# Optimization experiments

Measured on AMD Instinct MI355X. Metric: run time of the kernel, lower is better.

The kernel has to match this reference:

```python
import jax, jax.numpy as jnp
import numpy as np

CHUNK = 2048  # query points processed per step; bounds peak memory at [CHUNK, F, 3]


def _safe_div(num, den):
    den_s = jnp.where(jnp.abs(den) > 1e-12, den, 1.0)
    return num / den_s


def _closest_point_on_triangle(p, a, b, c):
    """Ericson's region-based closest point on triangle.
    p: [n,1,3], a/b/c: [1,F,3] -> returns [n,F,3]."""
    ab = b - a
    ac = c - a
    ap = p - a
    d1 = jnp.sum(ab * ap, -1)
    d2 = jnp.sum(ac * ap, -1)
    bp = p - b
    d3 = jnp.sum(ab * bp, -1)
    d4 = jnp.sum(ac * bp, -1)
    cpv = p - c
    d5 = jnp.sum(ab * cpv, -1)
    d6 = jnp.sum(ac * cpv, -1)
    vc = d1 * d4 - d3 * d2
    vb = d5 * d2 - d1 * d6
    va = d3 * d6 - d5 * d4
    v_ab = jnp.clip(_safe_div(d1, d1 - d3), 0.0, 1.0)
    w_ac = jnp.clip(_safe_div(d2, d2 - d6), 0.0, 1.0)
    w_bc = jnp.clip(_safe_div(d4 - d3, (d4 - d3) + (d5 - d6)), 0.0, 1.0)
    denom = va + vb + vc
    v = _safe_div(vb, denom)
    w = _safe_div(vc, denom)
    res = a + ab * v[..., None] + ac * w[..., None]  # face interior
    m_bc = (va <= 0) & ((d4 - d3) >= 0) & ((d5 - d6) >= 0)
    m_ac = (vb <= 0) & (d2 >= 0) & (d6 <= 0)
    m_ab = (vc <= 0) & (d1 >= 0) & (d3 <= 0)
    m_c = (d6 >= 0) & (d5 <= d6)
    m_b = (d3 >= 0) & (d4 <= d3)
    m_a = (d1 <= 0) & (d2 <= 0)
    res = jnp.where(m_bc[..., None], b + w_bc[..., None] * (c - b), res)
    res = jnp.where(m_ac[..., None], a + w_ac[..., None] * ac, res)
    res = jnp.where(m_ab[..., None], a + v_ab[..., None] * ab, res)
    res = jnp.where(m_c[..., None], c, res)
    res = jnp.where(m_b[..., None], b, res)
    res = jnp.where(m_a[..., None], a, res)
    return res


def _query_one_batch(tris, pts):
    # tris: [F,3,3], pts: [Q,3]
    a, b, c = tris[:, 0], tris[:, 1], tris[:, 2]

    def chunk_fn(pc):  # pc: [CHUNK,3]
        cp = _closest_point_on_triangle(pc[:, None, :], a[None], b[None], c[None])  # [CHUNK,F,3]
        d2 = jnp.sum((pc[:, None, :] - cp) ** 2, -1)  # [CHUNK,F] squared distances
        dist = jnp.min(d2, axis=-1)
        idx = jnp.argmin(d2, axis=-1)
        closest = jnp.take_along_axis(cp, idx[:, None, None], axis=1)[:, 0]
        return dist, closest, idx.astype(jnp.int32)

    Q = pts.shape[0]
    pts_c = pts.reshape(Q // CHUNK, CHUNK, 3)
    dist, closest, idx = jax.lax.map(chunk_fn, pts_c)
    return dist.reshape(Q), closest.reshape(Q, 3), idx.reshape(Q)


def setup_inputs() -> dict:
    key = jax.random.key(0)
    k1, k2 = jax.random.split(key)
    triangles = jax.random.normal(k1, (2, 4096, 3, 3), dtype=jnp.float32)
    points = jax.random.normal(k2, (2, 16384, 3), dtype=jnp.float32)
    return {"triangles": triangles, "points": points}


def reference(triangles, points):
    # distances are SQUARED point-to-mesh distances, matching the CUDA kernel
    distances, closest_points, closest_faces = jax.vmap(_query_one_batch)(triangles, points)
    return distances, closest_points, closest_faces
```

## Files before the change

kernel.cpp:

```cpp
#include <hip/hip_runtime.h>
#include <math.h>

namespace {

typedef float v2f __attribute__((ext_vector_type(2)));

constexpr int B = 2;
constexpr int F = 4096;
constexpr int Q = 16384;
constexpr int NP = B * Q;
constexpr int BLOCK = 256;
constexpr int P4 = 4;

constexpr int OFF_DIST = 0;
constexpr int OFF_CP = NP;
constexpr int OFF_FACE = 4 * NP;


__device__ __forceinline__ float safediv(float num, float den) {
  #pragma clang fp contract(off)
  float d = (fabsf(den) > 1e-12f) ? den : 1.0f;
  return num / d;
}

__device__ __forceinline__ float clamp01(float x) {
  return fminf(fmaxf(x, 0.0f), 1.0f);
}

__device__ __forceinline__ void closest_pt(
    float px, float py, float pz,
    float ax, float ay, float az,
    float bx, float by, float bz,
    float cx, float cy, float cz,
    float& rx, float& ry, float& rz) {
  #pragma clang fp contract(off)
  float abx = bx - ax, aby = by - ay, abz = bz - az;
  float acx = cx - ax, acy = cy - ay, acz = cz - az;
  float apx = px - ax, apy = py - ay, apz = pz - az;
  float d1 = (abx * apx + aby * apy) + abz * apz;
  float d2 = (acx * apx + acy * apy) + acz * apz;
  float bpx = px - bx, bpy = py - by, bpz = pz - bz;
  float d3 = (abx * bpx + aby * bpy) + abz * bpz;
  float d4 = (acx * bpx + acy * bpy) + acz * bpz;
  float cpx = px - cx, cpy = py - cy, cpz = pz - cz;
  float d5 = (abx * cpx + aby * cpy) + abz * cpz;
  float d6 = (acx * cpx + acy * cpy) + acz * cpz;

  float vc = d1 * d4 - d3 * d2;
  float vb = d5 * d2 - d1 * d6;
  float va = d3 * d6 - d5 * d4;

  float v_ab = clamp01(safediv(d1, d1 - d3));
  float w_ac = clamp01(safediv(d2, d2 - d6));
  float w_bc = clamp01(safediv(d4 - d3, (d4 - d3) + (d5 - d6)));

  float denom = (va + vb) + vc;
  float v = safediv(vb, denom);
  float w = safediv(vc, denom);

  float ox = ax + abx * v + acx * w;
  float oy = ay + aby * v + acy * w;
  float oz = az + abz * v + acz * w;

  bool m_bc = (va <= 0.0f) && (d4 - d3 >= 0.0f) && (d5 - d6 >= 0.0f);
  bool m_ac = (vb <= 0.0f) && (d2 >= 0.0f) && (d6 <= 0.0f);
  bool m_ab = (vc <= 0.0f) && (d1 >= 0.0f) && (d3 <= 0.0f);
  bool m_c  = (d6 >= 0.0f) && (d5 <= d6);
  bool m_b  = (d3 >= 0.0f) && (d4 <= d3);
  bool m_a  = (d1 <= 0.0f) && (d2 <= 0.0f);

  if (m_bc) { ox = bx + w_bc * (cx - bx); oy = by + w_bc * (cy - by); oz = bz + w_bc * (cz - bz); }
  if (m_ac) { ox = ax + w_ac * acx;       oy = ay + w_ac * acy;       oz = az + w_ac * acz; }
  if (m_ab) { ox = ax + v_ab * abx;       oy = ay + v_ab * aby;       oz = az + v_ab * abz; }
  if (m_c)  { ox = cx; oy = cy; oz = cz; }
  if (m_b)  { ox = bx; oy = by; oz = bz; }
  if (m_a)  { ox = ax; oy = ay; oz = az; }

  rx = ox; ry = oy; rz = oz;
}

__device__ __forceinline__ float exact_d2(
    float px, float py, float pz, const float* __restrict__ g ) {
  #pragma clang fp contract(off)
  float rx, ry, rz;
  closest_pt(px, py, pz,
             g[0], g[1], g[2], g[3], g[4], g[5], g[6], g[7], g[8],
             rx, ry, rz);
  float dx = px - rx, dy = py - ry, dz = pz - rz;
  return (dx * dx + dy * dy) + dz * dz;
}


__device__ __forceinline__ unsigned umin2(unsigned a, unsigned b) { return a < b ? a : b; }
__device__ __forceinline__ unsigned umax2(unsigned a, unsigned b) { return a > b ? a : b; }

__device__ __forceinline__ void ins2(unsigned k, unsigned& K1, unsigned& K2) {
  unsigned t = umax2(K1, k);
  K1 = umin2(K1, k);
  K2 = umin2(K2, t);
}

__device__ __forceinline__ void ins8(unsigned k,
    unsigned& K1, unsigned& K2, unsigned& K3, unsigned& K4,
    unsigned& K5, unsigned& K6, unsigned& K7, unsigned& K8) {
  unsigned t;
  t = umax2(K1, k); K1 = umin2(K1, k);
  k = t; t = umax2(K2, k); K2 = umin2(K2, k);
  k = t; t = umax2(K3, k); K3 = umin2(K3, k);
  k = t; t = umax2(K4, k); K4 = umin2(K4, k);
  k = t; t = umax2(K5, k); K5 = umin2(K5, k);
  k = t; t = umax2(K6, k); K6 = umin2(K6, k);
  k = t; t = umax2(K7, k); K7 = umin2(K7, k);
  K8 = umin2(K8, t);
}


__device__ __forceinline__ unsigned fin_one(
    float dint, float tabm, float tacm, float tbcm,
    float td1, float td2, float ap2m, float bp2, float t43d,
    float va, float vb, float vc,
    float aa, float bb, float cc, float pp, int gidx) {
  float tab = __builtin_amdgcn_fmed3f(tabm, 0.0f, 1.0f);
  float sab = fmaf(-tab, fmaf(-tab, aa, td1), ap2m);
  float tac = __builtin_amdgcn_fmed3f(tacm, 0.0f, 1.0f);
  float sac = fmaf(-tac, fmaf(-tac, bb, td2), ap2m);
  float tbc = __builtin_amdgcn_fmed3f(tbcm, 0.0f, 1.0f);
  float sbc = fmaf(-tbc, fmaf(-tbc, cc, t43d), bp2);
  float dseg = fminf(fminf(sab, sac), sbc);
  float mv   = fminf(fminf(va, vb), vc);
  float d = (mv > 0.0f) ? dint : dseg;
  d = fmaxf(d + pp, 0.0f);
  return (__float_as_uint(d) & 0xFFFFF000u) | (unsigned)gidx;
}

template <int NC>
__global__ __launch_bounds__(BLOCK, 4) void bvh_screen4(
    const float* __restrict__ tris,
    const float* __restrict__ pts,
    uint2* __restrict__ keys) {
  constexpr int CFL = F / NC;
  __shared__ float4 s_rec[5 * CFL];

  constexpr int BPB = (Q / P4) / BLOCK;
  const int batch = blockIdx.x / BPB;
  const int j = (blockIdx.x % BPB) * BLOCK + threadIdx.x;
  const int chunk = blockIdx.y;
  const int tri0 = chunk * CFL;
  const float* tb = tris + (size_t)batch * F * 9;

  for (int t = threadIdx.x; t < CFL; t += BLOCK) {
    const float* g = tb + (size_t)(tri0 + t) * 9;
    float ax = g[0], ay = g[1], az = g[2];
    float abx = g[3] - ax, aby = g[4] - ay, abz = g[5] - az;
    float acx = g[6] - ax, acy = g[7] - ay, acz = g[8] - az;
    float aa   = abx * abx + aby * aby + abz * abz;
    float bb   = acx * acx + acy * acy + acz * acz;
    float abac = abx * acx + aby * acy + abz * acz;
    float bcx = acx - abx, bcy = acy - aby, bcz = acz - abz;
    float cc   = bcx * bcx + bcy * bcy + bcz * bcz;
    float nx = aby * acz - abz * acy;
    float ny = abz * acx - abx * acz;
    float nz = abx * acy - aby * acx;
    float n2 = nx * nx + ny * ny + nz * nz;
    float raa = (aa > 1e-12f) ? 1.0f / aa : 1.0f;
    float rbb = (bb > 1e-12f) ? 1.0f / bb : 1.0f;
    float rcc = (cc > 1e-12f) ? 1.0f / cc : 1.0f;
    float rdn = (n2 > 1e-12f) ? 1.0f / n2 : 1.0f;
    float c1 = -(ax * abx + ay * aby + az * abz);
    float c2 = -(ax * acx + ay * acy + az * acz);
    float caa2 = ax * ax + ay * ay + az * az;
    s_rec[0 * CFL + t] = make_float4(abx, aby, abz, c1);
    s_rec[1 * CFL + t] = make_float4(acx, acy, acz, c2);
    s_rec[2 * CFL + t] = make_float4(-2.0f * ax, -2.0f * ay, -2.0f * az, caa2);
    s_rec[3 * CFL + t] = make_float4(aa, bb, abac, cc);
    s_rec[4 * CFL + t] = make_float4(raa, rbb, rcc, rdn);
  }
  __syncthreads();

  const int p0 = batch * Q + j;
  float px0 = pts[(p0          ) * 3 + 0], py0 = pts[(p0          ) * 3 + 1], pz0 = pts[(p0          ) * 3 + 2];
  float px1 = pts[(p0 + Q/4    ) * 3 + 0], py1 = pts[(p0 + Q/4    ) * 3 + 1], pz1 = pts[(p0 + Q/4    ) * 3 + 2];
  float px2 = pts[(p0 + Q/2    ) * 3 + 0], py2 = pts[(p0 + Q/2    ) * 3 + 1], pz2 = pts[(p0 + Q/2    ) * 3 + 2];
  float px3 = pts[(p0 + 3*(Q/4)) * 3 + 0], py3 = pts[(p0 + 3*(Q/4)) * 3 + 1], pz3 = pts[(p0 + 3*(Q/4)) * 3 + 2];

  const v2f pxA = {px0, px1}, pyA = {py0, py1}, pzA = {pz0, pz1};
  const v2f pxB = {px2, px3}, pyB = {py2, py3}, pzB = {pz2, pz3};
  const float pp0 = px0*px0 + py0*py0 + pz0*pz0;
  const float pp1 = px1*px1 + py1*py1 + pz1*pz1;
  const float pp2 = px2*px2 + py2*py2 + pz2*pz2;
  const float pp3 = px3*px3 + py3*py3 + pz3*pz3;

  unsigned A1 = ~0u, A2 = ~0u, Bk1 = ~0u, Bk2 = ~0u;
  unsigned C1 = ~0u, C2 = ~0u, D1 = ~0u, D2 = ~0u;

  {
    #pragma clang fp contract(fast)
    for (int t = 0; t < CFL; ++t) {
      const float4 R0 = s_rec[0 * CFL + t];
      const float4 R1 = s_rec[1 * CFL + t];
      const float4 R2 = s_rec[2 * CFL + t];
      const float4 R3 = s_rec[3 * CFL + t];
      const float4 R4 = s_rec[4 * CFL + t];
      const int gidx = tri0 + t;

      {
        v2f d1   = pxA * R0.x + pyA * R0.y + pzA * R0.z + R0.w;
        v2f d2   = pxA * R1.x + pyA * R1.y + pzA * R1.z + R1.w;
        v2f ap2m = pxA * R2.x + pyA * R2.y + pzA * R2.z + R2.w;
        v2f d3 = d1 - R3.x, d6 = d2 - R3.y, d4 = d2 - R3.z, d5 = d1 - R3.z;
        v2f t43 = d4 - d3;
        v2f va = d3 * d6 - d5 * d4;
        v2f vb = d5 * d2 - d1 * d6;
        v2f vc = d1 * d4 - d3 * d2;
        v2f td1 = d1 + d1, td2 = d2 + d2;
        v2f v = vb * R4.w, w = vc * R4.w;
        v2f h1 = v * R3.x + (w * R3.z - td1);
        v2f h2 = w * R3.y + (v * R3.z - td2);
        v2f dint = ap2m + (v * h1 + w * h2);
        v2f tabm = d1 * R4.x, tacm = d2 * R4.y, tbcm = t43 * R4.z;
        v2f bp2 = (ap2m - td1) + R3.x;
        v2f t43d = t43 + t43;
        ins2(fin_one(dint.x, tabm.x, tacm.x, tbcm.x, td1.x, td2.x, ap2m.x,
                     bp2.x, t43d.x, va.x, vb.x, vc.x,
                     R3.x, R3.y, R3.w, pp0, gidx), A1, A2);
        ins2(fin_one(dint.y, tabm.y, tacm.y, tbcm.y, td1.y, td2.y, ap2m.y,
                     bp2.y, t43d.y, va.y, vb.y, vc.y,
                     R3.x, R3.y, R3.w, pp1, gidx), Bk1, Bk2);
      }
      {
        v2f d1   = pxB * R0.x + pyB * R0.y + pzB * R0.z + R0.w;
        v2f d2   = pxB * R1.x + pyB * R1.y + pzB * R1.z + R1.w;
        v2f ap2m = pxB * R2.x + pyB * R2.y + pzB * R2.z + R2.w;
        v2f d3 = d1 - R3.x, d6 = d2 - R3.y, d4 = d2 - R3.z, d5 = d1 - R3.z;
        v2f t43 = d4 - d3;
        v2f va = d3 * d6 - d5 * d4;
        v2f vb = d5 * d2 - d1 * d6;
        v2f vc = d1 * d4 - d3 * d2;
        v2f td1 = d1 + d1, td2 = d2 + d2;
        v2f v = vb * R4.w, w = vc * R4.w;
        v2f h1 = v * R3.x + (w * R3.z - td1);
        v2f h2 = w * R3.y + (v * R3.z - td2);
        v2f dint = ap2m + (v * h1 + w * h2);
        v2f tabm = d1 * R4.x, tacm = d2 * R4.y, tbcm = t43 * R4.z;
        v2f bp2 = (ap2m - td1) + R3.x;
        v2f t43d = t43 + t43;
        ins2(fin_one(dint.x, tabm.x, tacm.x, tbcm.x, td1.x, td2.x, ap2m.x,
                     bp2.x, t43d.x, va.x, vb.x, vc.x,
                     R3.x, R3.y, R3.w, pp2, gidx), C1, C2);
        ins2(fin_one(dint.y, tabm.y, tacm.y, tbcm.y, td1.y, td2.y, ap2m.y,
                     bp2.y, t43d.y, va.y, vb.y, vc.y,
                     R3.x, R3.y, R3.w, pp3, gidx), D1, D2);
      }
    }
  }

  keys[(size_t)chunk * NP + p0            ] = make_uint2(A1, A2);
  keys[(size_t)chunk * NP + p0 + Q/4      ] = make_uint2(Bk1, Bk2);
  keys[(size_t)chunk * NP + p0 + Q/2      ] = make_uint2(C1, C2);
  keys[(size_t)chunk * NP + p0 + 3*(Q/4)  ] = make_uint2(D1, D2);
}


template <int NC>
__global__ __launch_bounds__(BLOCK) void bvh_finish2(
    const float* __restrict__ tris,
    const float* __restrict__ pts,
    const uint2* __restrict__ keys,
    float* __restrict__ out) {
  const int gpt = blockIdx.x * BLOCK + threadIdx.x;
  if (gpt >= NP) return;

  unsigned K1 = ~0u, K2 = ~0u, K3 = ~0u, K4 = ~0u;
  unsigned K5 = ~0u, K6 = ~0u, K7 = ~0u, K8 = ~0u;
  for (int c = 0; c < NC; ++c) {
    uint2 k = keys[(size_t)c * NP + gpt];
    ins8(k.x, K1, K2, K3, K4, K5, K6, K7, K8);
    ins8(k.y, K1, K2, K3, K4, K5, K6, K7, K8);
  }

  const int batch = gpt / Q;
  const float* tb = tris + (size_t)batch * F * 9;
  const float px = pts[gpt * 3 + 0];
  const float py = pts[gpt * 3 + 1];
  const float pz = pts[gpt * 3 + 2];

  float be = INFINITY;
  int bi = 0x7FFFFFFF;
  #define CAND(Kx) { int t_ = (int)(Kx & 0xFFFu); \
    float d_ = exact_d2(px, py, pz, tb + (size_t)t_ * 9); \
    if (d_ < be || (d_ == be && t_ < bi)) { be = d_; bi = t_; } }
  CAND(K1) CAND(K2) CAND(K3) CAND(K4) CAND(K5) CAND(K6) CAND(K7) CAND(K8)
  #undef CAND

  const float* tr = tb + (size_t)bi * 9;
  float rx, ry, rz;
  closest_pt(px, py, pz,
             tr[0], tr[1], tr[2], tr[3], tr[4], tr[5], tr[6], tr[7], tr[8],
             rx, ry, rz);

  out[OFF_DIST + gpt] = be;
  out[OFF_CP + gpt * 3 + 0] = rx;
  out[OFF_CP + gpt * 3 + 1] = ry;
  out[OFF_CP + gpt * 3 + 2] = rz;
  out[OFF_FACE + gpt] = (float)bi;
}


__device__ __forceinline__ float screen_d2_sc(
    float px, float py, float pz,
    float ax, float ay, float az,
    float abx, float aby, float abz,
    float acx, float acy, float acz,
    float aa, float bb, float abac,
    float raa, float rbb, float rcc, float rdn) {
  #pragma clang fp contract(fast)
  float apx = px - ax, apy = py - ay, apz = pz - az;
  float ap2 = fmaf(apx, apx, fmaf(apy, apy, apz * apz));
  float d1  = fmaf(apx, abx, fmaf(apy, aby, apz * abz));
  float d2  = fmaf(apx, acx, fmaf(apy, acy, apz * acz));
  float d3 = d1 - aa, d6 = d2 - bb, d4 = d2 - abac, d5 = d1 - abac;
  float t43 = d4 - d3, t56 = d5 - d6;
  float va = d3 * d6 - d5 * d4;
  float vb = d5 * d2 - d1 * d6;
  float vc = d1 * d4 - d3 * d2;
  float td1 = d1 + d1, td2 = d2 + d2;
  float v = vb * rdn, w = vc * rdn;
  float h1 = fmaf(v, aa, fmaf(w, abac, -td1));
  float h2 = fmaf(w, bb, fmaf(v, abac, -td2));
  float dint = ap2 + fmaf(v, h1, w * h2);
  float tab = __builtin_amdgcn_fmed3f(d1 * raa, 0.0f, 1.0f);
  float sab = fmaf(-tab, fmaf(-tab, aa, td1), ap2);
  float tac = __builtin_amdgcn_fmed3f(d2 * rbb, 0.0f, 1.0f);
  float sac = fmaf(-tac, fmaf(-tac, bb, td2), ap2);
  float cc  = t43 + t56;
  float bp2 = (ap2 - td1) + aa;
  float tbc = __builtin_amdgcn_fmed3f(t43 * rcc, 0.0f, 1.0f);
  float sbc = fmaf(-tbc, fmaf(-tbc, cc, t43 + t43), bp2);
  float dseg = fminf(fminf(sab, sac), sbc);
  float mv   = fminf(fminf(va, vb), vc);
  float d = (mv > 0.0f) ? dint : dseg;
  return fmaxf(d, 0.0f);
}

__device__ __forceinline__ void ins4c(unsigned key,
    unsigned& K1, unsigned& K2, unsigned& K3, unsigned& K4) {
  bool b1 = key < K1, b2 = key < K2, b3 = key < K3, b4 = key < K4;
  K4 = b3 ? K3 : (b4 ? key : K4);
  K3 = b2 ? K2 : (b3 ? key : K3);
  K2 = b1 ? K1 : (b2 ? key : K2);
  K1 = b1 ? key : K1;
}

__device__ __forceinline__ void tail4(
    const float* __restrict__ tb, int tri0,
    float px, float py, float pz,
    unsigned K1, unsigned K2, unsigned K3, unsigned K4,
    float& be, int& bi) {
  int c0 = (int)(K1 & 0x1FFu), c1 = (int)(K2 & 0x1FFu);
  int c2 = (int)(K3 & 0x1FFu), c3 = (int)(K4 & 0x1FFu);
  int tmp;
  if (c0 > c1) { tmp = c0; c0 = c1; c1 = tmp; }
  if (c2 > c3) { tmp = c2; c2 = c3; c3 = tmp; }
  if (c0 > c2) { tmp = c0; c0 = c2; c2 = tmp; }
  if (c1 > c3) { tmp = c1; c1 = c3; c3 = tmp; }
  if (c1 > c2) { tmp = c1; c1 = c2; c2 = tmp; }
  be = exact_d2(px, py, pz, tb + (size_t)(tri0 + c0) * 9);
  bi = c0;
  { float d = exact_d2(px, py, pz, tb + (size_t)(tri0 + c1) * 9);
    if (d < be) { be = d; bi = c1; } }
  { float d = exact_d2(px, py, pz, tb + (size_t)(tri0 + c2) * 9);
    if (d < be) { be = d; bi = c2; } }
  { float d = exact_d2(px, py, pz, tb + (size_t)(tri0 + c3) * 9);
    if (d < be) { be = d; bi = c3; } }
}

template <int NC>
__global__ __launch_bounds__(BLOCK, 4) void bvh_partial_p2(
    const float* __restrict__ tris,
    const float* __restrict__ pts,
    float* __restrict__ dbest,
    unsigned short* __restrict__ ibest) {
  constexpr int CFL = F / NC;
  __shared__ float4 s_rec[4 * CFL];

  constexpr int BPB = (Q / 2) / BLOCK;
  const int batch = blockIdx.x / BPB;
  const int j = (blockIdx.x % BPB) * BLOCK + threadIdx.x;
  const int chunk = blockIdx.y;
  const int tri0 = chunk * CFL;
  const float* tb = tris + (size_t)batch * F * 9;

  for (int t = threadIdx.x; t < CFL; t += BLOCK) {
    const float* g = tb + (size_t)(tri0 + t) * 9;
    float ax = g[0], ay = g[1], az = g[2];
    float abx = g[3] - ax, aby = g[4] - ay, abz = g[5] - az;
    float acx = g[6] - ax, acy = g[7] - ay, acz = g[8] - az;
    float aa   = abx * abx + aby * aby + abz * abz;
    float bb   = acx * acx + acy * acy + acz * acz;
    float abac = abx * acx + aby * acy + abz * acz;
    float bcx = acx - abx, bcy = acy - aby, bcz = acz - abz;
    float cc   = bcx * bcx + bcy * bcy + bcz * bcz;
    float nx = aby * acz - abz * acy;
    float ny = abz * acx - abx * acz;
    float nz = abx * acy - aby * acx;
    float n2 = nx * nx + ny * ny + nz * nz;
    float raa = (aa > 1e-12f) ? 1.0f / aa : 1.0f;
    float rbb = (bb > 1e-12f) ? 1.0f / bb : 1.0f;
    float rcc = (cc > 1e-12f) ? 1.0f / cc : 1.0f;
    float rdn = (n2 > 1e-12f) ? 1.0f / n2 : 1.0f;
    s_rec[0 * CFL + t] = make_float4(ax, ay, az, abx);
    s_rec[1 * CFL + t] = make_float4(aby, abz, acx, acy);
    s_rec[2 * CFL + t] = make_float4(acz, aa, bb, abac);
    s_rec[3 * CFL + t] = make_float4(raa, rbb, rcc, rdn);
  }
  __syncthreads();

  const int p0 = batch * Q + j;
  const int p1 = p0 + Q / 2;
  const float px0 = pts[p0 * 3 + 0], py0 = pts[p0 * 3 + 1], pz0 = pts[p0 * 3 + 2];
  const float px1 = pts[p1 * 3 + 0], py1 = pts[p1 * 3 + 1], pz1 = pts[p1 * 3 + 2];

  unsigned A1 = ~0u, A2 = ~0u, A3 = ~0u, A4 = ~0u;
  unsigned B1 = ~0u, B2 = ~0u, B3 = ~0u, B4 = ~0u;

  for (int t = 0; t < CFL; ++t) {
    const float4 R0 = s_rec[0 * CFL + t];
    const float4 R1 = s_rec[1 * CFL + t];
    const float4 R2 = s_rec[2 * CFL + t];
    const float4 R3 = s_rec[3 * CFL + t];
    float ax = R0.x, ay = R0.y, az = R0.z, abx = R0.w;
    float aby = R1.x, abz = R1.y, acx = R1.z, acy = R1.w;
    float acz = R2.x, aa = R2.y, bb = R2.z, abac = R2.w;
    float raa = R3.x, rbb = R3.y, rcc = R3.z, rdn = R3.w;

    float d0 = screen_d2_sc(px0, py0, pz0, ax, ay, az, abx, aby, abz,
                            acx, acy, acz, aa, bb, abac, raa, rbb, rcc, rdn);
    ins4c((__float_as_uint(d0) & 0xFFFFFE00u) | (unsigned)t, A1, A2, A3, A4);
    float d1 = screen_d2_sc(px1, py1, pz1, ax, ay, az, abx, aby, abz,
                            acx, acy, acz, aa, bb, abac, raa, rbb, rcc, rdn);
    ins4c((__float_as_uint(d1) & 0xFFFFFE00u) | (unsigned)t, B1, B2, B3, B4);
  }

  float be0, be1;
  int bi0, bi1;
  tail4(tb, tri0, px0, py0, pz0, A1, A2, A3, A4, be0, bi0);
  tail4(tb, tri0, px1, py1, pz1, B1, B2, B3, B4, be1, bi1);

  dbest[chunk * NP + p0] = be0;
  ibest[chunk * NP + p0] = (unsigned short)(tri0 + bi0);
  dbest[chunk * NP + p1] = be1;
  ibest[chunk * NP + p1] = (unsigned short)(tri0 + bi1);
}

template <int NC>
__global__ __launch_bounds__(BLOCK) void bvh_reduce(
    const float* __restrict__ tris,
    const float* __restrict__ pts,
    const float* __restrict__ dbest,
    const unsigned short* __restrict__ ibest,
    float* __restrict__ out) {
  const int gpt = blockIdx.x * BLOCK + threadIdx.x;
  if (gpt >= NP) return;

  float best = INFINITY;
  int bi = 0;
  for (int c = 0; c < NC; ++c) {
    float d = dbest[c * NP + gpt];
    if (d < best) { best = d; bi = ibest[c * NP + gpt]; }
  }

  const int batch = gpt / Q;
  const float px = pts[gpt * 3 + 0];
  const float py = pts[gpt * 3 + 1];
  const float pz = pts[gpt * 3 + 2];

  const float* tr = tris + ((size_t)batch * F + bi) * 9;
  float rx, ry, rz;
  closest_pt(px, py, pz,
             tr[0], tr[1], tr[2], tr[3], tr[4], tr[5], tr[6], tr[7], tr[8],
             rx, ry, rz);

  out[OFF_DIST + gpt] = best;
  out[OFF_CP + gpt * 3 + 0] = rx;
  out[OFF_CP + gpt * 3 + 1] = ry;
  out[OFF_CP + gpt * 3 + 2] = rz;
  out[OFF_FACE + gpt] = (float)bi;
}

}

extern "C" void kernel_launch(void* const* d_in, const int* in_sizes, int n_in,
                              void* d_out, int out_size, void* d_ws, size_t ws_size,
                              hipStream_t stream) {
  const float* tris = (const float*)d_in[0];
  const float* pts  = (const float*)d_in[1];
  float* out = (float*)d_out;

  dim3 grid2((NP + BLOCK - 1) / BLOCK);

  constexpr int NC = 32;
  constexpr size_t KEY_BYTES = (size_t)NC * NP * sizeof(uint2);

  if (ws_size >= KEY_BYTES) {
    uint2* keys = (uint2*)d_ws;
    const int gx = B * ((Q / P4) / BLOCK);
    bvh_screen4<NC><<<dim3(gx, NC), BLOCK, 0, stream>>>(tris, pts, keys);
    bvh_finish2<NC><<<grid2, BLOCK, 0, stream>>>(tris, pts, keys, out);
  } else {
    float* dbest = (float*)d_ws;
    unsigned short* ibest = (unsigned short*)((char*)d_ws + (size_t)8 * NP * sizeof(float));
    const int gx = B * ((Q / 2) / BLOCK);
    bvh_partial_p2<8><<<dim3(gx, 8), BLOCK, 0, stream>>>(tris, pts, dbest, ibest);
    bvh_reduce<8><<<grid2, BLOCK, 0, stream>>>(tris, pts, dbest, ibest, out);
  }
}
```

Baseline: 166.8 us.

## Precompute triangle records in a prep kernel and read them from global memory

Adds a bvh_prep kernel that computes the per-triangle records once for all batches and writes them to workspace. The screening kernel now reads these records directly from global memory with uniform loads instead of rebuilding them into shared memory in every block, and its loop is unrolled by 2. This removes the per-block setup work and the barrier, but costs an extra launch and per-iteration global or cache loads in place of LDS reads. The old two-point fallback path is replaced by the shared-memory screen kernel.

New measurement: 172.1 us. 3.2% more time.

```diff
diff --git a/kernel.cpp b/kernel.cpp
--- a/kernel.cpp
+++ b/kernel.cpp
@@ -114,7 +114,6 @@
   K8 = umin2(K8, t);
 }
 
-
 __device__ __forceinline__ unsigned fin_one(
     float dint, float tabm, float tacm, float tbcm,
     float td1, float td2, float ap2m, float bp2, float t43d,
@@ -133,49 +132,52 @@
   return (__float_as_uint(d) & 0xFFFFF000u) | (unsigned)gidx;
 }
 
+
+__global__ __launch_bounds__(BLOCK) void bvh_prep(
+    const float* __restrict__ tris, float4* __restrict__ rec) {
+  int i = blockIdx.x * BLOCK + threadIdx.x;
+  if (i >= B * F) return;
+  const float* g = tris + (size_t)i * 9;
+  float ax = g[0], ay = g[1], az = g[2];
+  float abx = g[3] - ax, aby = g[4] - ay, abz = g[5] - az;
+  float acx = g[6] - ax, acy = g[7] - ay, acz = g[8] - az;
+  float aa   = abx * abx + aby * aby + abz * abz;
+  float bb   = acx * acx + acy * acy + acz * acz;
+  float abac = abx * acx + aby * acy + abz * acz;
+  float bcx = acx - abx, bcy = acy - aby, bcz = acz - abz;
+  float cc   = bcx * bcx + bcy * bcy + bcz * bcz;
+  float nx = aby * acz - abz * acy;
+  float ny = abz * acx - abx * acz;
+  float nz = abx * acy - aby * acx;
+  float n2 = nx * nx + ny * ny + nz * nz;
+  float raa = (aa > 1e-12f) ? 1.0f / aa : 1.0f;
+  float rbb = (bb > 1e-12f) ? 1.0f / bb : 1.0f;
+  float rcc = (cc > 1e-12f) ? 1.0f / cc : 1.0f;
+  float rdn = (n2 > 1e-12f) ? 1.0f / n2 : 1.0f;
+  float c1 = -(ax * abx + ay * aby + az * abz);
+  float c2 = -(ax * acx + ay * acy + az * acz);
+  float caa2 = ax * ax + ay * ay + az * az;
+  float4* r = rec + (size_t)i * 5;
+  r[0] = make_float4(abx, aby, abz, c1);
+  r[1] = make_float4(acx, acy, acz, c2);
+  r[2] = make_float4(-2.0f * ax, -2.0f * ay, -2.0f * az, caa2);
+  r[3] = make_float4(aa, bb, abac, cc);
+  r[4] = make_float4(raa, rbb, rcc, rdn);
+}
+
+
 template <int NC>
-__global__ __launch_bounds__(BLOCK, 4) void bvh_screen4(
-    const float* __restrict__ tris,
+__global__ __launch_bounds__(BLOCK, 4) void bvh_screen_smem(
     const float* __restrict__ pts,
+    const float4* __restrict__ rec,
     uint2* __restrict__ keys) {
   constexpr int CFL = F / NC;
-  __shared__ float4 s_rec[5 * CFL];
-
   constexpr int BPB = (Q / P4) / BLOCK;
   const int batch = blockIdx.x / BPB;
   const int j = (blockIdx.x % BPB) * BLOCK + threadIdx.x;
   const int chunk = blockIdx.y;
   const int tri0 = chunk * CFL;
-  const float* tb = tris + (size_t)batch * F * 9;
-
-  for (int t = threadIdx.x; t < CFL; t += BLOCK) {
-    const float* g = tb + (size_t)(tri0 + t) * 9;
-    float ax = g[0], ay = g[1], az = g[2];
-    float abx = g[3] - ax, aby = g[4] - ay, abz = g[5] - az;
-    float acx = g[6] - ax, acy = g[7] - ay, acz = g[8] - az;
-    float aa   = abx * abx + aby * aby + abz * abz;
-    float bb   = acx * acx + acy * acy + acz * acz;
-    float abac = abx * acx + aby * acy + abz * acz;
-    float bcx = acx - abx, bcy = acy - aby, bcz = acz - abz;
-    float cc   = bcx * bcx + bcy * bcy + bcz * bcz;
-    float nx = aby * acz - abz * acy;
-    float ny = abz * acx - abx * acz;
-    float nz = abx * acy - aby * acx;
-    float n2 = nx * nx + ny * ny + nz * nz;
-    float raa = (aa > 1e-12f) ? 1.0f / aa : 1.0f;
-    float rbb = (bb > 1e-12f) ? 1.0f / bb : 1.0f;
-    float rcc = (cc > 1e-12f) ? 1.0f / cc : 1.0f;
-    float rdn = (n2 > 1e-12f) ? 1.0f / n2 : 1.0f;
-    float c1 = -(ax * abx + ay * aby + az * abz);
-    float c2 = -(ax * acx + ay * acy + az * acz);
-    float caa2 = ax * ax + ay * ay + az * az;
-    s_rec[0 * CFL + t] = make_float4(abx, aby, abz, c1);
-    s_rec[1 * CFL + t] = make_float4(acx, acy, acz, c2);
-    s_rec[2 * CFL + t] = make_float4(-2.0f * ax, -2.0f * ay, -2.0f * az, caa2);
-    s_rec[3 * CFL + t] = make_float4(aa, bb, abac, cc);
-    s_rec[4 * CFL + t] = make_float4(raa, rbb, rcc, rdn);
-  }
-  __syncthreads();
+  const float4* rb = rec + ((size_t)batch * F + tri0) * 5;
 
   const int p0 = batch * Q + j;
   float px0 = pts[(p0          ) * 3 + 0], py0 = pts[(p0          ) * 3 + 1], pz0 = pts[(p0          ) * 3 + 2];
@@ -195,12 +197,13 @@
 
   {
     #pragma clang fp contract(fast)
+    #pragma unroll 2
     for (int t = 0; t < CFL; ++t) {
-      const float4 R0 = s_rec[0 * CFL + t];
-      const float4 R1 = s_rec[1 * CFL + t];
-      const float4 R2 = s_rec[2 * CFL + t];
-      const float4 R3 = s_rec[3 * CFL + t];
-      const float4 R4 = s_rec[4 * CFL + t];
+      const float4 R0 = rb[t * 5 + 0];
+      const float4 R1 = rb[t * 5 + 1];
+      const float4 R2 = rb[t * 5 + 2];
+      const float4 R3 = rb[t * 5 + 3];
+      const float4 R4 = rb[t * 5 + 4];
       const int gidx = tri0 + t;
 
       {
@@ -306,84 +309,15 @@
 }
 
 
-__device__ __forceinline__ float screen_d2_sc(
-    float px, float py, float pz,
-    float ax, float ay, float az,
-    float abx, float aby, float abz,
-    float acx, float acy, float acz,
-    float aa, float bb, float abac,
-    float raa, float rbb, float rcc, float rdn) {
-  #pragma clang fp contract(fast)
-  float apx = px - ax, apy = py - ay, apz = pz - az;
-  float ap2 = fmaf(apx, apx, fmaf(apy, apy, apz * apz));
-  float d1  = fmaf(apx, abx, fmaf(apy, aby, apz * abz));
-  float d2  = fmaf(apx, acx, fmaf(apy, acy, apz * acz));
-  float d3 = d1 - aa, d6 = d2 - bb, d4 = d2 - abac, d5 = d1 - abac;
-  float t43 = d4 - d3, t56 = d5 - d6;
-  float va = d3 * d6 - d5 * d4;
-  float vb = d5 * d2 - d1 * d6;
-  float vc = d1 * d4 - d3 * d2;
-  float td1 = d1 + d1, td2 = d2 + d2;
-  float v = vb * rdn, w = vc * rdn;
-  float h1 = fmaf(v, aa, fmaf(w, abac, -td1));
-  float h2 = fmaf(w, bb, fmaf(v, abac, -td2));
-  float dint = ap2 + fmaf(v, h1, w * h2);
-  float tab = __builtin_amdgcn_fmed3f(d1 * raa, 0.0f, 1.0f);
-  float sab = fmaf(-tab, fmaf(-tab, aa, td1), ap2);
-  float tac = __builtin_amdgcn_fmed3f(d2 * rbb, 0.0f, 1.0f);
-  float sac = fmaf(-tac, fmaf(-tac, bb, td2), ap2);
-  float cc  = t43 + t56;
-  float bp2 = (ap2 - td1) + aa;
-  float tbc = __builtin_amdgcn_fmed3f(t43 * rcc, 0.0f, 1.0f);
-  float sbc = fmaf(-tbc, fmaf(-tbc, cc, t43 + t43), bp2);
-  float dseg = fminf(fminf(sab, sac), sbc);
-  float mv   = fminf(fminf(va, vb), vc);
-  float d = (mv > 0.0f) ? dint : dseg;
-  return fmaxf(d, 0.0f);
-}
-
-__device__ __forceinline__ void ins4c(unsigned key,
-    unsigned& K1, unsigned& K2, unsigned& K3, unsigned& K4) {
-  bool b1 = key < K1, b2 = key < K2, b3 = key < K3, b4 = key < K4;
-  K4 = b3 ? K3 : (b4 ? key : K4);
-  K3 = b2 ? K2 : (b3 ? key : K3);
-  K2 = b1 ? K1 : (b2 ? key : K2);
-  K1 = b1 ? key : K1;
-}
-
-__device__ __forceinline__ void tail4(
-    const float* __restrict__ tb, int tri0,
-    float px, float py, float pz,
-    unsigned K1, unsigned K2, unsigned K3, unsigned K4,
-    float& be, int& bi) {
-  int c0 = (int)(K1 & 0x1FFu), c1 = (int)(K2 & 0x1FFu);
-  int c2 = (int)(K3 & 0x1FFu), c3 = (int)(K4 & 0x1FFu);
-  int tmp;
-  if (c0 > c1) { tmp = c0; c0 = c1; c1 = tmp; }
-  if (c2 > c3) { tmp = c2; c2 = c3; c3 = tmp; }
-  if (c0 > c2) { tmp = c0; c0 = c2; c2 = tmp; }
-  if (c1 > c3) { tmp = c1; c1 = c3; c3 = tmp; }
-  if (c1 > c2) { tmp = c1; c1 = c2; c2 = tmp; }
-  be = exact_d2(px, py, pz, tb + (size_t)(tri0 + c0) * 9);
-  bi = c0;
-  { float d = exact_d2(px, py, pz, tb + (size_t)(tri0 + c1) * 9);
-    if (d < be) { be = d; bi = c1; } }
-  { float d = exact_d2(px, py, pz, tb + (size_t)(tri0 + c2) * 9);
-    if (d < be) { be = d; bi = c2; } }
-  { float d = exact_d2(px, py, pz, tb + (size_t)(tri0 + c3) * 9);
-    if (d < be) { be = d; bi = c3; } }
-}
-
 template <int NC>
-__global__ __launch_bounds__(BLOCK, 4) void bvh_partial_p2(
+__global__ __launch_bounds__(BLOCK, 4) void bvh_screen4(
     const float* __restrict__ tris,
     const float* __restrict__ pts,
-    float* __restrict__ dbest,
-    unsigned short* __restrict__ ibest) {
+    uint2* __restrict__ keys) {
   constexpr int CFL = F / NC;
-  __shared__ float4 s_rec[4 * CFL];
-
-  constexpr int BPB = (Q / 2) / BLOCK;
+  __shared__ float4 s_rec[5 * CFL];
+
+  constexpr int BPB = (Q / P4) / BLOCK;
   const int batch = blockIdx.x / BPB;
   const int j = (blockIdx.x % BPB) * BLOCK + threadIdx.x;
   const int chunk = blockIdx.y;
@@ -408,83 +342,97 @@
     float rbb = (bb > 1e-12f) ? 1.0f / bb : 1.0f;
     float rcc = (cc > 1e-12f) ? 1.0f / cc : 1.0f;
     float rdn = (n2 > 1e-12f) ? 1.0f / n2 : 1.0f;
-    s_rec[0 * CFL + t] = make_float4(ax, ay, az, abx);
-    s_rec[1 * CFL + t] = make_float4(aby, abz, acx, acy);
-    s_rec[2 * CFL + t] = make_float4(acz, aa, bb, abac);
-    s_rec[3 * CFL + t] = make_float4(raa, rbb, rcc, rdn);
+    float c1 = -(ax * abx + ay * aby + az * abz);
+    float c2 = -(ax * acx + ay * acy + az * acz);
+    float caa2 = ax * ax + ay * ay + az * az;
+    s_rec[0 * CFL + t] = make_float4(abx, aby, abz, c1);
+    s_rec[1 * CFL + t] = make_float4(acx, acy, acz, c2);
+    s_rec[2 * CFL + t] = make_float4(-2.0f * ax, -2.0f * ay, -2.0f * az, caa2);
+    s_rec[3 * CFL + t] = make_float4(aa, bb, abac, cc);
+    s_rec[4 * CFL + t] = make_float4(raa, rbb, rcc, rdn);
   }
   __syncthreads();
 
   const int p0 = batch * Q + j;
-  const int p1 = p0 + Q / 2;
-  const float px0 = pts[p0 * 3 + 0], py0 = pts[p0 * 3 + 1], pz0 = pts[p0 * 3 + 2];
-  const float px1 = pts[p1 * 3 + 0], py1 = pts[p1 * 3 + 1], pz1 = pts[p1 * 3 + 2];
-
-  unsigned A1 = ~0u, A2 = ~0u, A3 = ~0u, A4 = ~0u;
-  unsigned B1 = ~0u, B2 = ~0u, B3 = ~0u, B4 = ~0u;
-
-  for (int t = 0; t < CFL; ++t) {
-    const float4 R0 = s_rec[0 * CFL + t];
-    const float4 R1 = s_rec[1 * CFL + t];
-    const float4 R2 = s_rec[2 * CFL + t];
-    const float4 R3 = s_rec[3 * CFL + t];
-    float ax = R0.x, ay = R0.y, az = R0.z, abx = R0.w;
-    float aby = R1.x, abz = R1.y, acx = R1.z, acy = R1.w;
-    float acz = R2.x, aa = R2.y, bb = R2.z, abac = R2.w;
-    float raa = R3.x, rbb = R3.y, rcc = R3.z, rdn = R3.w;
-
-    float d0 = screen_d2_sc(px0, py0, pz0, ax, ay, az, abx, aby, abz,
-                            acx, acy, acz, aa, bb, abac, raa, rbb, rcc, rdn);
-    ins4c((__float_as_uint(d0) & 0xFFFFFE00u) | (unsigned)t, A1, A2, A3, A4);
-    float d1 = screen_d2_sc(px1, py1, pz1, ax, ay, az, abx, aby, abz,
-                            acx, acy, acz, aa, bb, abac, raa, rbb, rcc, rdn);
-    ins4c((__float_as_uint(d1) & 0xFFFFFE00u) | (unsigned)t, B1, B2, B3, B4);
+  float px0 = pts[(p0          ) * 3 + 0], py0 = pts[(p0          ) * 3 + 1], pz0 = pts[(p0          ) * 3 + 2];
+  float px1 = pts[(p0 + Q/4    ) * 3 + 0], py1 = pts[(p0 + Q/4    ) * 3 + 1], pz1 = pts[(p0 + Q/4    ) * 3 + 2];
+  float px2 = pts[(p0 + Q/2    ) * 3 + 0], py2 = pts[(p0 + Q/2    ) * 3 + 1], pz2 = pts[(p0 + Q/2    ) * 3 + 2];
+  float px3 = pts[(p0 + 3*(Q/4)) * 3 + 0], py3 = pts[(p0 + 3*(Q/4)) * 3 + 1], pz3 = pts[(p0 + 3*(Q/4)) * 3 + 2];
+
+  const v2f pxA = {px0, px1}, pyA = {py0, py1}, pzA = {pz0, pz1};
+  const v2f pxB = {px2, px3}, pyB = {py2, py3}, pzB = {pz2, pz3};
+  const float pp0 = px0*px0 + py0*py0 + pz0*pz0;
+  const float pp1 = px1*px1 + py1*py1 + pz1*pz1;
+  const float pp2 = px2*px2 + py2*py2 + pz2*pz2;
+  const float pp3 = px3*px3 + py3*py3 + pz3*pz3;
+
+  unsigned A1 = ~0u, A2 = ~0u, Bk1 = ~0u, Bk2 = ~0u;
+  unsigned C1 = ~0u, C2 = ~0u, D1 = ~0u, D2 = ~0u;
+
+  {
+    #pragma clang fp contract(fast)
+    for (int t = 0; t < CFL; ++t) {
+      const float4 R0 = s_rec[0 * CFL + t];
+      const float4 R1 = s_rec[1 * CFL + t];
+      const float4 R2 = s_rec[2 * CFL + t];
+      const float4 R3 = s_rec[3 * CFL + t];
+      const float4 R4 = s_rec[4 * CFL + t];
+      const int gidx = tri0 + t;
+      {
+        v2f d1   = pxA * R0.x + pyA * R0.y + pzA * R0.z + R0.w;
+        v2f d2   = pxA * R1.x + pyA * R1.y + pzA * R1.z + R1.w;
+        v2f ap2m = pxA * R2.x + pyA * R2.y + pzA * R2.z + R2.w;
+        v2f d3 = d1 - R3.x, d6 = d2 - R3.y, d4 = d2 - R3.z, d5 = d1 - R3.z;
+        v2f t43 = d4 - d3;
+        v2f va = d3 * d6 - d5 * d4;
+        v2f vb = d5 * d2 - d1 * d6;
+        v2f vc = d1 * d4 - d3 * d2;
+        v2f td1 = d1 + d1, td2 = d2 + d2;
+        v2f v = vb * R4.w, w = vc * R4.w;
+        v2f h1 = v * R3.x + (w * R3.z - td1);
+        v2f h2 = w * R3.y + (v * R3.z - td2);
+        v2f dint = ap2m + (v * h1 + w * h2);
+        v2f tabm = d1 * R4.x, tacm = d2 * R4.y, tbcm = t43 * R4.z;
+        v2f bp2 = (ap2m - td1) + R3.x;
+        v2f t43d = t43 + t43;
+        ins2(fin_one(dint.x, tabm.x, tacm.x, tbcm.x, td1.x, td2.x, ap2m.x,
+                     bp2.x, t43d.x, va.x, vb.x, vc.x,
+                     R3.x, R3.y, R3.w, pp0, gidx), A1, A2);
+        ins2(fin_one(dint.y, tabm.y, tacm.y, tbcm.y, td1.y, td2.y, ap2m.y,
+                     bp2.y, t43d.y, va.y, vb.y, vc.y,
+                     R3.x, R3.y, R3.w, pp1, gidx), Bk1, Bk2);
+      }
+      {
+        v2f d1   = pxB * R0.x + pyB * R0.y + pzB * R0.z + R0.w;
+        v2f d2   = pxB * R1.x + pyB * R1.y + pzB * R1.z + R1.w;
+        v2f ap2m = pxB * R2.x + pyB * R2.y + pzB * R2.z + R2.w;
+        v2f d3 = d1 - R3.x, d6 = d2 - R3.y, d4 = d2 - R3.z, d5 = d1 - R3.z;
+        v2f t43 = d4 - d3;
+        v2f va = d3 * d6 - d5 * d4;
+        v2f vb = d5 * d2 - d1 * d6;
+        v2f vc = d1 * d4 - d3 * d2;
+        v2f td1 = d1 + d1, td2 = d2 + d2;
+        v2f v = vb * R4.w, w = vc * R4.w;
+        v2f h1 = v * R3.x + (w * R3.z - td1);
+        v2f h2 = w * R3.y + (v * R3.z - td2);
+        v2f dint = ap2m + (v * h1 + w * h2);
+        v2f tabm = d1 * R4.x, tacm = d2 * R4.y, tbcm = t43 * R4.z;
+        v2f bp2 = (ap2m - td1) + R3.x;
+        v2f t43d = t43 + t43;
+        ins2(fin_one(dint.x, tabm.x, tacm.x, tbcm.x, td1.x, td2.x, ap2m.x,
+                     bp2.x, t43d.x, va.x, vb.x, vc.x,
+                     R3.x, R3.y, R3.w, pp2, gidx), C1, C2);
+        ins2(fin_one(dint.y, tabm.y, tacm.y, tbcm.y, td1.y, td2.y, ap2m.y,
+                     bp2.y, t43d.y, va.y, vb.y, vc.y,
+                     R3.x, R3.y, R3.w, pp3, gidx), D1, D2);
+      }
+    }
   }
 
-  float be0, be1;
-  int bi0, bi1;
-  tail4(tb, tri0, px0, py0, pz0, A1, A2, A3, A4, be0, bi0);
-  tail4(tb, tri0, px1, py1, pz1, B1, B2, B3, B4, be1, bi1);
-
-  dbest[chunk * NP + p0] = be0;
-  ibest[chunk * NP + p0] = (unsigned short)(tri0 + bi0);
-  dbest[chunk * NP + p1] = be1;
-  ibest[chunk * NP + p1] = (unsigned short)(tri0 + bi1);
-}
-
-template <int NC>
-__global__ __launch_bounds__(BLOCK) void bvh_reduce(
-    const float* __restrict__ tris,
-    const float* __restrict__ pts,
-    const float* __restrict__ dbest,
-    const unsigned short* __restrict__ ibest,
-    float* __restrict__ out) {
-  const int gpt = blockIdx.x * BLOCK + threadIdx.x;
-  if (gpt >= NP) return;
-
-  float best = INFINITY;
-  int bi = 0;
-  for (int c = 0; c < NC; ++c) {
-    float d = dbest[c * NP + gpt];
-    if (d < best) { best = d; bi = ibest[c * NP + gpt]; }
-  }
-
-  const int batch = gpt / Q;
-  const float px = pts[gpt * 3 + 0];
-  const float py = pts[gpt * 3 + 1];
-  const float pz = pts[gpt * 3 + 2];
-
-  const float* tr = tris + ((size_t)batch * F + bi) * 9;
-  float rx, ry, rz;
-  closest_pt(px, py, pz,
-             tr[0], tr[1], tr[2], tr[3], tr[4], tr[5], tr[6], tr[7], tr[8],
-             rx, ry, rz);
-
-  out[OFF_DIST + gpt] = best;
-  out[OFF_CP + gpt * 3 + 0] = rx;
-  out[OFF_CP + gpt * 3 + 1] = ry;
-  out[OFF_CP + gpt * 3 + 2] = rz;
-  out[OFF_FACE + gpt] = (float)bi;
+  keys[(size_t)chunk * NP + p0            ] = make_uint2(A1, A2);
+  keys[(size_t)chunk * NP + p0 + Q/4      ] = make_uint2(Bk1, Bk2);
+  keys[(size_t)chunk * NP + p0 + Q/2      ] = make_uint2(C1, C2);
+  keys[(size_t)chunk * NP + p0 + 3*(Q/4)  ] = make_uint2(D1, D2);
 }
 
 }
@@ -500,17 +448,18 @@
 
   constexpr int NC = 32;
   constexpr size_t KEY_BYTES = (size_t)NC * NP * sizeof(uint2);
-
-  if (ws_size >= KEY_BYTES) {
+  constexpr size_t REC_BYTES = (size_t)B * F * 5 * sizeof(float4);
+  const int gx = B * ((Q / P4) / BLOCK);
+
+  if (ws_size >= KEY_BYTES + REC_BYTES) {
     uint2* keys = (uint2*)d_ws;
-    const int gx = B * ((Q / P4) / BLOCK);
+    float4* rec = (float4*)((char*)d_ws + KEY_BYTES);
+    bvh_prep<<<(B * F + BLOCK - 1) / BLOCK, BLOCK, 0, stream>>>(tris, rec);
+    bvh_screen_smem<NC><<<dim3(gx, NC), BLOCK, 0, stream>>>(pts, rec, keys);
+    bvh_finish2<NC><<<grid2, BLOCK, 0, stream>>>(tris, pts, keys, out);
+  } else {
+    uint2* keys = (uint2*)d_ws;
     bvh_screen4<NC><<<dim3(gx, NC), BLOCK, 0, stream>>>(tris, pts, keys);
     bvh_finish2<NC><<<grid2, BLOCK, 0, stream>>>(tris, pts, keys, out);
-  } else {
-    float* dbest = (float*)d_ws;
-    unsigned short* ibest = (unsigned short*)((char*)d_ws + (size_t)8 * NP * sizeof(float));
-    const int gx = B * ((Q / 2) / BLOCK);
-    bvh_partial_p2<8><<<dim3(gx, 8), BLOCK, 0, stream>>>(tris, pts, dbest, ibest);
-    bvh_reduce<8><<<grid2, BLOCK, 0, stream>>>(tris, pts, dbest, ibest, out);
   }
 }
```
